# Kernel tuning notes

Hardware: AMD Instinct MI355X
Metric: run time of the kernel (lower is better)

The kernel has to match this reference:

```python
import jax, jax.numpy as jnp
import numpy as np

D_MODEL = 256
N_LEVELS = 4
N_HEADS = 8
N_POINTS = 4
OFF_DIM = 32
D_HEAD = D_MODEL // N_HEADS
SHAPES = [(64, 64), (32, 32), (16, 16), (8, 8)]  # (H_l, W_l)
LEN_IN = sum(h * w for h, w in SHAPES)  # 5440
N_BATCH = 4
LEN_Q = LEN_IN


def _offset_bias_init():
    # replicates _reset_parameters grid_init for sampling_offsets_bias
    thetas = np.arange(N_HEADS, dtype=np.float32) * (2.0 * np.pi / N_HEADS)
    grid = np.stack([np.cos(thetas), np.sin(thetas)], -1)
    grid = grid / np.abs(grid).max(-1, keepdims=True)
    grid = np.tile(grid[:, None, None, :], (1, N_LEVELS, N_POINTS, 1))
    grid = grid * np.arange(1, N_POINTS + 1, dtype=np.float32)[None, None, :, None]
    return jnp.asarray(grid, jnp.float32)  # (H, L, K, 2)


def setup_inputs() -> dict:
    key = jax.random.key(0)
    ks = jax.random.split(key, 12)
    s = 0.02
    return {
        "query": jax.random.normal(ks[0], (N_BATCH, LEN_Q, D_MODEL), jnp.float32),
        "reference_points": jax.random.uniform(ks[1], (N_BATCH, LEN_Q, N_LEVELS, 2), jnp.float32),
        "input_flatten": jax.random.normal(ks[2], (N_BATCH, LEN_IN, D_MODEL), jnp.float32),
        "input_spatial_shapes": jnp.asarray(SHAPES, jnp.int32),
        "offset_embeds_W": jax.random.normal(ks[3], (N_HEADS * N_LEVELS * N_POINTS * OFF_DIM, D_MODEL), jnp.float32) * s,
        "sampling_offsets_W": jax.random.normal(ks[4], (N_HEADS, N_LEVELS, N_POINTS, OFF_DIM, 2), jnp.float32) * s,
        "sampling_offsets_b": _offset_bias_init(),
        "attn_W": jax.random.normal(ks[5], (N_HEADS, N_LEVELS, N_POINTS, OFF_DIM, 1), jnp.float32) * s,
        "attn_b": jax.random.normal(ks[6], (N_HEADS, N_LEVELS, N_POINTS), jnp.float32) * s,
        "value_W": jax.random.normal(ks[7], (D_MODEL, D_MODEL), jnp.float32) * (1.0 / np.sqrt(D_MODEL)),
        "value_b": jnp.zeros((D_MODEL,), jnp.float32),
        "out_W": jax.random.normal(ks[8], (D_MODEL, D_MODEL), jnp.float32) * (1.0 / np.sqrt(D_MODEL)),
        "out_b": jnp.zeros((D_MODEL,), jnp.float32),
    }


def _bilinear(v, loc, H, W):
    # v: (N, heads, H*W, d_head); loc: (N, Lq, heads, K, 2) in [0,1] (x=width, y=height)
    # matches torch grid_sample(mode=bilinear, padding=zeros, align_corners=False)
    N, Lq, Hh, K, _ = loc.shape
    x = loc[..., 0] * W - 0.5
    y = loc[..., 1] * H - 0.5
    x0 = jnp.floor(x)
    y0 = jnp.floor(y)
    wx = (x - x0).transpose(0, 2, 1, 3).reshape(N, Hh, Lq * K)[..., None]
    wy = (y - y0).transpose(0, 2, 1, 3).reshape(N, Hh, Lq * K)[..., None]
    x0i = x0.astype(jnp.int32)
    y0i = y0.astype(jnp.int32)

    def gather(xi, yi):
        valid = (xi >= 0) & (xi < W) & (yi >= 0) & (yi < H)
        idx = jnp.clip(yi, 0, H - 1) * W + jnp.clip(xi, 0, W - 1)
        idx = idx.transpose(0, 2, 1, 3).reshape(N, Hh, Lq * K)
        g = jnp.take_along_axis(v, idx[..., None], axis=2)  # (N, heads, Lq*K, d)
        m = valid.transpose(0, 2, 1, 3).reshape(N, Hh, Lq * K)
        return g * m[..., None].astype(v.dtype)

    g00 = gather(x0i, y0i)
    g01 = gather(x0i + 1, y0i)
    g10 = gather(x0i, y0i + 1)
    g11 = gather(x0i + 1, y0i + 1)
    out = (g00 * (1 - wx) * (1 - wy) + g01 * wx * (1 - wy)
           + g10 * (1 - wx) * wy + g11 * wx * wy)
    return out.reshape(N, Hh, Lq, K, -1)  # (N, heads, Lq, K, d_head)


def _forward(query, reference_points, input_flatten,
             offset_embeds_W, sampling_offsets_W, sampling_offsets_b,
             attn_W, attn_b, value_W, value_b, out_W, out_b):
    N, Lq, _ = query.shape
    # value projection
    value = input_flatten @ value_W.T + value_b                      # (N, Lin, C)
    value = value.reshape(N, -1, N_HEADS, D_HEAD)                    # (N, Lin, H, d)

    # offset embedding + activation (offset_act_name == 'silu')
    oe = jax.nn.silu(query @ offset_embeds_W.T)                      # (N, Lq, H*L*K*off)
    oe = oe.reshape(N, Lq, N_HEADS, N_LEVELS, N_POINTS, OFF_DIM)

    offs = jnp.einsum('bqhlkd,hlkdc->bqhlkc', oe, sampling_offsets_W) + sampling_offsets_b
    aw = jnp.einsum('bqhlkd,hlkd->bqhlk', oe, attn_W[..., 0]) + attn_b
    aw = jax.nn.softmax(aw.reshape(N, Lq, N_HEADS, N_LEVELS * N_POINTS), axis=-1)
    aw = aw.reshape(N, Lq, N_HEADS, N_LEVELS, N_POINTS)

    # normalize offsets by (W_l, H_l) and add reference points (2-dim branch)
    normalizer = jnp.asarray([[w, h] for h, w in SHAPES], jnp.float32)  # (L, 2)
    loc = reference_points[:, :, None, :, None, :] + offs / normalizer[None, None, None, :, None, :]

    out = jnp.zeros((N, Lq, N_HEADS, D_HEAD), jnp.float32)
    start = 0
    for lvl, (H, W) in enumerate(SHAPES):
        v_l = value[:, start:start + H * W].transpose(0, 2, 1, 3)    # (N, heads, HW, d)
        sampled = _bilinear(v_l, loc[:, :, :, lvl], H, W)            # (N, heads, Lq, K, d)
        out = out + jnp.einsum('bhqkd,bqhk->bqhd', sampled, aw[:, :, :, lvl])
        start += H * W
    out = out.reshape(N, Lq, D_MODEL)
    return out @ out_W.T + out_b


def reference(query, reference_points, input_flatten, input_spatial_shapes,
              offset_embeds_W, sampling_offsets_W, sampling_offsets_b,
              attn_W, attn_b, value_W, value_b, out_W, out_b):
    # input_spatial_shapes matches SHAPES (static pyramid)
    return _forward(query, reference_points, input_flatten,
                    offset_embeds_W, sampling_offsets_W, sampling_offsets_b,
                    attn_W, attn_b, value_W, value_b, out_W, out_b)
```

## Files before the change

### kernel.cpp

```cpp
#include <hip/hip_runtime.h>
#include <hip/hip_bf16.h>

#define NB 4
#define LQ 5440
#define DM 256
#define NH 8
#define NL 4
#define NP 4
#define OFFD 32
#define DH 32
#define MTOT (NB * LQ)
#define OEN (NH * NL * NP * OFFD)
#define NGRP (NH * NL * NP)

typedef __attribute__((ext_vector_type(8))) short bf16x8;
typedef __attribute__((ext_vector_type(4))) float f32x4;
typedef unsigned int u32;

#define GLOAD_LDS16(gp, lp) \
    __builtin_amdgcn_global_load_lds((const __attribute__((address_space(1))) u32*)(gp), \
                                     (__attribute__((address_space(3))) u32*)(lp), 16, 0, 0)

__device__ __forceinline__ float bf2f(unsigned short u) {
    union { unsigned int i; float f; } v; v.i = ((unsigned int)u) << 16; return v.f;
}
__device__ __forceinline__ unsigned short f2bf(float x) {
    u32 u = __float_as_uint(x);
    u = u + 0x7fffu + ((u >> 16) & 1u);
    return (unsigned short)(u >> 16);
}
__device__ __forceinline__ u32 pk2(float a, float b) {
    u32 ua = __float_as_uint(a), ub = __float_as_uint(b);
    ua = ua + 0x7fffu + ((ua >> 16) & 1u);
    ub = ub + 0x7fffu + ((ub >> 16) & 1u);
    return (ua >> 16) | (ub & 0xffff0000u);
}
__device__ __forceinline__ float silu(float x) {
    float e = __expf(-x);
    return x * __builtin_amdgcn_rcpf(1.0f + e);
}

__global__ __launch_bounds__(256) void k_cvt2(
    const float* __restrict__ A, unsigned short* __restrict__ Ao,
    const float* __restrict__ B, unsigned short* __restrict__ Bo, int n4)
{
    int i = blockIdx.x * 256 + threadIdx.x;
    if (i >= n4) return;
    const float* src = blockIdx.y ? B : A;
    unsigned short* dst = blockIdx.y ? Bo : Ao;
    float4 v = *(const float4*)(src + (size_t)i * 4);
    ushort4 o;
    o.x = f2bf(v.x); o.y = f2bf(v.y); o.z = f2bf(v.z); o.w = f2bf(v.w);
    *(ushort4*)(dst + (size_t)i * 4) = o;
}
__global__ __launch_bounds__(256) void k_cvt3(
    const float* __restrict__ A, unsigned short* __restrict__ Ao, int nA4,
    const float* __restrict__ B, unsigned short* __restrict__ Bo, int nB4,
    const float* __restrict__ C, unsigned short* __restrict__ Co, int nC4,
    const float* __restrict__ SW, const float* __restrict__ AW,
    unsigned short* __restrict__ Rb)
{
    int i = blockIdx.x * 256 + threadIdx.x;
    if (blockIdx.y == 3) {
        if (i < 65536) {
            int gg = i >> 9, jo = (i >> 5) & 15, d = i & 31;
            float v = 0.f;
            if (jo == 0)      v = SW[(gg * 32 + d) * 2 + 0];
            else if (jo == 1) v = SW[(gg * 32 + d) * 2 + 1];
            else if (jo == 2) v = AW[gg * 32 + d];
            Rb[i] = f2bf(v);
        }
        return;
    }
    const float* src; unsigned short* dst; int n4;
    if (blockIdx.y == 0)      { src = A; dst = Ao; n4 = nA4; }
    else if (blockIdx.y == 1) { src = B; dst = Bo; n4 = nB4; }
    else                      { src = C; dst = Co; n4 = nC4; }
    if (i >= n4) return;
    float4 v = *(const float4*)(src + (size_t)i * 4);
    ushort4 o;
    o.x = f2bf(v.x); o.y = f2bf(v.y); o.z = f2bf(v.z); o.w = f2bf(v.w);
    *(ushort4*)(dst + (size_t)i * 4) = o;
}

__global__ __launch_bounds__(256) void k_oe_mfma(
    const unsigned short* __restrict__ Qb,
    const unsigned short* __restrict__ Wb,
    const unsigned short* __restrict__ Rb,
    const float* __restrict__ SB,
    const float* __restrict__ AB,
    float* __restrict__ offs_out,
    float* __restrict__ aw_out)
{
    __shared__ short sA[128 * 64];
    __shared__ short sB[128 * 64];
    int tid = threadIdx.x;
    int n0 = blockIdx.x * 128;
    int m0 = blockIdx.y * 128;

    int lane = tid & 63;
    int w = tid >> 6;
    int wA = w >> 1;
    int wB = w & 1;
    int lcol = lane & 15, quad = lane >> 4;

    int srow = tid >> 3;
    int sq = (tid & 7) ^ (srow & 7);
    const short* gA = (const short*)Qb + (size_t)(m0 + srow) * 256 + sq * 8;
    const short* gB = (const short*)Wb + (size_t)(n0 + srow) * 256 + sq * 8;
    short* lA = sA + w * 512;
    short* lB = sB + w * 512;

    f32x4 acc[4][4] = {};

    const short* pq = sA + (wB * 64 + lcol) * 64;
    const short* pw = sB + (wA * 64 + lcol) * 64;
    int rx7 = lcol & 7;
    int qa0 = (quad ^ rx7) * 8;
    int qa1 = ((4 + quad) ^ rx7) * 8;

    for (int kc = 0; kc < 256; kc += 64) {
#pragma unroll
        for (int j = 0; j < 4; j++) {
            GLOAD_LDS16(gA + kc + j * 32 * 256, lA + j * 2048);
            GLOAD_LDS16(gB + kc + j * 32 * 256, lB + j * 2048);
        }
        __syncthreads();
        bf16x8 a[4][2], b[4][2];
#pragma unroll
        for (int i = 0; i < 4; i++) {
            a[i][0] = *(const bf16x8*)(pw + i * 16 * 64 + qa0);
            a[i][1] = *(const bf16x8*)(pw + i * 16 * 64 + qa1);
            b[i][0] = *(const bf16x8*)(pq + i * 16 * 64 + qa0);
            b[i][1] = *(const bf16x8*)(pq + i * 16 * 64 + qa1);
        }
#pragma unroll
        for (int kh = 0; kh < 2; kh++)
#pragma unroll
            for (int i = 0; i < 4; i++)
#pragma unroll
                for (int j = 0; j < 4; j++)
                    acc[i][j] = __builtin_amdgcn_mfma_f32_16x16x32_bf16(
                        a[i][kh], b[j][kh], acc[i][j], 0, 0, 0);
        __syncthreads();
    }

    u32 ps[4][4][2];
#pragma unroll
    for (int i = 0; i < 4; i++)
#pragma unroll
        for (int j = 0; j < 4; j++) {
            ps[i][j][0] = pk2(silu(acc[i][j][0]), silu(acc[i][j][1]));
            ps[i][j][1] = pk2(silu(acc[i][j][2]), silu(acc[i][j][3]));
        }

    int srcbase = (quad & 1) * 32 + lcol;
    bool hi = quad >= 2;
    f32x4 zero = {};
#pragma unroll
    for (int g = 0; g < 2; g++) {
        int gg = (n0 + wA * 64 + g * 32) >> 5;
        bf16x8 afrag = *(const bf16x8*)(Rb + ((size_t)(gg * 16 + lcol) * 32 + quad * 8));
        float sb0 = SB[gg * 2 + 0], sb1 = SB[gg * 2 + 1], ab = AB[gg];
#pragma unroll
        for (int j = 0; j < 4; j++) {
            union { u32 u[4]; bf16x8 v; } bf;
#pragma unroll
            for (int b = 0; b < 2; b++) {
                int s = srcbase + b * 16;
#pragma unroll
                for (int c = 0; c < 2; c++) {
                    u32 x0 = (u32)__shfl((int)ps[2 * g + 0][j][c], s);
                    u32 x1 = (u32)__shfl((int)ps[2 * g + 1][j][c], s);
                    bf.u[b * 2 + c] = hi ? x1 : x0;
                }
            }
            f32x4 d2 = __builtin_amdgcn_mfma_f32_16x16x32_bf16(afrag, bf.v, zero, 0, 0, 0);
            if (quad == 0) {
                int m = m0 + wB * 64 + j * 16 + lcol;
                size_t oi = ((size_t)m * NGRP + gg) * 2;
                offs_out[oi + 0] = d2[0] + sb0;
                offs_out[oi + 1] = d2[1] + sb1;
                aw_out[(size_t)m * NGRP + gg] = d2[2] + ab;
            }
        }
    }
}

__global__ __launch_bounds__(256) void k_value_mfma(
    const unsigned short* __restrict__ Xb,
    const unsigned short* __restrict__ Wvb,
    const float* __restrict__ bias,
    unsigned short* __restrict__ Vtb)
{
    __shared__ short sA[128 * 64];
    __shared__ short sB[128 * 64];
    int tid = threadIdx.x;
    int n0 = blockIdx.x * 128;
    int m0 = blockIdx.y * 128;
    int lane = tid & 63;
    int w = tid >> 6;
    int wA = w >> 1;
    int wB = w & 1;
    int lcol = lane & 15, quad = lane >> 4;

    int srow = tid >> 3;
    int sq = (tid & 7) ^ (srow & 7);
    const short* gA = (const short*)Xb + (size_t)(m0 + srow) * 256 + sq * 8;
    const short* gB = (const short*)Wvb + (size_t)(n0 + srow) * 256 + sq * 8;
    short* lA = sA + w * 512;
    short* lB = sB + w * 512;

    f32x4 acc[4][4] = {};
    const short* px = sA + (wB * 64 + lcol) * 64;
    const short* pw = sB + (wA * 64 + lcol) * 64;
    int rx7 = lcol & 7;
    int qa0 = (quad ^ rx7) * 8;
    int qa1 = ((4 + quad) ^ rx7) * 8;

    for (int kc = 0; kc < 256; kc += 64) {
#pragma unroll
        for (int j = 0; j < 4; j++) {
            GLOAD_LDS16(gA + kc + j * 32 * 256, lA + j * 2048);
            GLOAD_LDS16(gB + kc + j * 32 * 256, lB + j * 2048);
        }
        __syncthreads();
        bf16x8 a[4][2], b[4][2];
#pragma unroll
        for (int i = 0; i < 4; i++) {
            a[i][0] = *(const bf16x8*)(pw + i * 16 * 64 + qa0);
            a[i][1] = *(const bf16x8*)(pw + i * 16 * 64 + qa1);
            b[i][0] = *(const bf16x8*)(px + i * 16 * 64 + qa0);
            b[i][1] = *(const bf16x8*)(px + i * 16 * 64 + qa1);
        }
#pragma unroll
        for (int kh = 0; kh < 2; kh++)
#pragma unroll
            for (int i = 0; i < 4; i++)
#pragma unroll
                for (int j = 0; j < 4; j++)
                    acc[i][j] = __builtin_amdgcn_mfma_f32_16x16x32_bf16(
                        a[i][kh], b[j][kh], acc[i][j], 0, 0, 0);
        __syncthreads();
    }

#pragma unroll
    for (int i = 0; i < 4; i++) {
        int nb = n0 + wA * 64 + i * 16 + quad * 4;
        int h = nb >> 5, db = nb & 31;
        float4 b4 = *(const float4*)&bias[nb];
#pragma unroll
        for (int j = 0; j < 4; j++) {
            int m = m0 + wB * 64 + j * 16 + lcol;
            int b = m / LQ, q = m - b * LQ;
            u32 lo = pk2(acc[i][j][0] + b4.x, acc[i][j][1] + b4.y);
            u32 hi2 = pk2(acc[i][j][2] + b4.z, acc[i][j][3] + b4.w);
            char* dst = (char*)Vtb + ((((size_t)b * NH + h) * LQ + q) * DH + db) * 2;
            *(uint2*)dst = make_uint2(lo, hi2);
        }
    }
}

__global__ __launch_bounds__(256) void k_out_mfma(
    const unsigned short* __restrict__ Xb,
    const unsigned short* __restrict__ Wob,
    const float* __restrict__ bias,
    float* __restrict__ Out)
{
    __shared__ short sA[128 * 64];
    __shared__ short sB[128 * 64];
    int tid = threadIdx.x;
    int n0 = blockIdx.x * 128;
    int m0 = blockIdx.y * 128;
    int lane = tid & 63;
    int w = tid >> 6;
    int wm = w >> 1, wn = w & 1;
    int lcol = lane & 15, lrow = lane >> 4;

    int srow = tid >> 3;
    int sq = (tid & 7) ^ (srow & 7);
    const short* gA = (const short*)Xb + (size_t)(m0 + srow) * 256 + sq * 8;
    const short* gB = (const short*)Wob + (size_t)(n0 + srow) * 256 + sq * 8;
    short* lA = sA + w * 512;
    short* lB = sB + w * 512;

    f32x4 acc[4][4] = {};
    const short* pa = sA + (wm * 64 + lcol) * 64;
    const short* pb = sB + (wn * 64 + lcol) * 64;
    int rx7 = lcol & 7;
    int qa0 = (lrow ^ rx7) * 8;
    int qa1 = ((4 + lrow) ^ rx7) * 8;

    for (int kc = 0; kc < 256; kc += 64) {
#pragma unroll
        for (int j = 0; j < 4; j++) {
            GLOAD_LDS16(gA + kc + j * 32 * 256, lA + j * 2048);
            GLOAD_LDS16(gB + kc + j * 32 * 256, lB + j * 2048);
        }
        __syncthreads();
        bf16x8 a[4][2], b[4][2];
#pragma unroll
        for (int i = 0; i < 4; i++) {
            a[i][0] = *(const bf16x8*)(pa + i * 16 * 64 + qa0);
            a[i][1] = *(const bf16x8*)(pa + i * 16 * 64 + qa1);
            b[i][0] = *(const bf16x8*)(pb + i * 16 * 64 + qa0);
            b[i][1] = *(const bf16x8*)(pb + i * 16 * 64 + qa1);
        }
#pragma unroll
        for (int kh = 0; kh < 2; kh++)
#pragma unroll
            for (int mi = 0; mi < 4; mi++)
#pragma unroll
                for (int ni = 0; ni < 4; ni++)
                    acc[mi][ni] = __builtin_amdgcn_mfma_f32_16x16x32_bf16(
                        a[mi][kh], b[ni][kh], acc[mi][ni], 0, 0, 0);
        __syncthreads();
    }

#pragma unroll
    for (int mi = 0; mi < 4; mi++) {
#pragma unroll
        for (int ni = 0; ni < 4; ni++) {
            int n = n0 + wn * 64 + ni * 16 + lcol;
            float bn = bias[n];
#pragma unroll
            for (int r = 0; r < 4; r++) {
                int m = m0 + wm * 64 + mi * 16 + lrow * 4 + r;
                Out[(size_t)m * 256 + n] = acc[mi][ni][r] + bn;
            }
        }
    }
}

__global__ __launch_bounds__(256) void k_sample(
    const unsigned short* __restrict__ Vtb,
    const float* __restrict__ refp,
    const float* __restrict__ offs,
    const float* __restrict__ awl,
    unsigned short* __restrict__ atnb)
{
    int tid = threadIdx.x;
    int m_base = blockIdx.x * 4;
    __shared__ int2 s_iw[4][128][4];

#pragma unroll
    for (int rep = 0; rep < 2; rep++) {
        int p = tid & 127;
        int mloc = (tid >> 7) + rep * 2;
        int m = m_base + mloc;
        int l = (p >> 2) & 3;
        float logit = awl[(size_t)m * 128 + p];
        float mx = logit;
#pragma unroll
        for (int off = 1; off < 16; off <<= 1) mx = fmaxf(mx, __shfl_xor(mx, off));
        float e = __expf(logit - mx);
        float s = e;
#pragma unroll
        for (int off = 1; off < 16; off <<= 1) s += __shfl_xor(s, off);
        float prob = e * __builtin_amdgcn_rcpf(s);

        float ox = offs[((size_t)m * 128 + p) * 2 + 0];
        float oy = offs[((size_t)m * 128 + p) * 2 + 1];
        float rx = refp[(size_t)m * 8 + l * 2 + 0];
        float ry = refp[(size_t)m * 8 + l * 2 + 1];
        int Wl = 64 >> l;
        int base = (l == 0) ? 0 : (l == 1) ? 4096 : (l == 2) ? 5120 : 5376;
        float fW = (float)Wl;
        float x = rx * fW + ox - 0.5f;
        float y = ry * fW + oy - 0.5f;
        float x0f = floorf(x), y0f = floorf(y);
        float wx = x - x0f, wy = y - y0f;
        int x0 = (int)x0f, y0 = (int)y0f;
        int xc0 = min(max(x0, 0), Wl - 1), xc1 = min(max(x0 + 1, 0), Wl - 1);
        int yc0 = min(max(y0, 0), Wl - 1), yc1 = min(max(y0 + 1, 0), Wl - 1);
        float vx0 = (x0 >= 0 && x0 < Wl) ? 1.f : 0.f;
        float vx1 = (x0 + 1 < Wl) ? 1.f : 0.f;
        float vy0 = (y0 >= 0 && y0 < Wl) ? 1.f : 0.f;
        float vy1 = (y0 + 1 < Wl) ? 1.f : 0.f;
        if (x0 + 1 < 0) vx1 = 0.f;
        if (y0 + 1 < 0) vy1 = 0.f;
        s_iw[mloc][p][0] = make_int2((base + yc0 * Wl + xc0) * 64,
                                     __float_as_int(prob * (1.f - wx) * (1.f - wy) * vx0 * vy0));
        s_iw[mloc][p][1] = make_int2((base + yc0 * Wl + xc1) * 64,
                                     __float_as_int(prob * wx * (1.f - wy) * vx1 * vy0));
        s_iw[mloc][p][2] = make_int2((base + yc1 * Wl + xc0) * 64,
                                     __float_as_int(prob * (1.f - wx) * wy * vx0 * vy1));
        s_iw[mloc][p][3] = make_int2((base + yc1 * Wl + xc1) * 64,
                                     __float_as_int(prob * wx * wy * vx1 * vy1));
    }
    __syncthreads();

    int wv = tid >> 6, lane = tid & 63;
    int p8 = lane >> 3, seg = lane & 7;
    int m = m_base + wv;
    int b = m / LQ;
    const char* vB = (const char*)(Vtb + (size_t)b * NH * LQ * DH) + seg * 8;
#pragma unroll
    for (int h = 0; h < 8; h++) {
        const char* ph = vB + (size_t)h * (LQ * DH * 2);
        float a0 = 0.f, a1 = 0.f, a2 = 0.f, a3 = 0.f;
#pragma unroll
        for (int pg = 0; pg < 2; pg++) {
            int p = h * 16 + pg * 8 + p8;
#pragma unroll
            for (int c = 0; c < 4; c++) {
                int2 iw = s_iw[wv][p][c];
                uint2 v = *(const uint2*)(ph + iw.x);
                float wgt = __int_as_float(iw.y);
                a0 += wgt * __uint_as_float(v.x << 16);
                a1 += wgt * __uint_as_float(v.x & 0xffff0000u);
                a2 += wgt * __uint_as_float(v.y << 16);
                a3 += wgt * __uint_as_float(v.y & 0xffff0000u);
            }
        }
#pragma unroll
        for (int off = 8; off <= 32; off <<= 1) {
            a0 += __shfl_xor(a0, off);
            a1 += __shfl_xor(a1, off);
            a2 += __shfl_xor(a2, off);
            a3 += __shfl_xor(a3, off);
        }
        if (p8 == 0) {
            ((uint2*)atnb)[(size_t)m * 64 + h * 8 + seg] =
                make_uint2(pk2(a0, a1), pk2(a2, a3));
        }
    }
}

extern "C" void kernel_launch(void* const* d_in, const int* in_sizes, int n_in,
                              void* d_out, int out_size, void* d_ws, size_t ws_size,
                              hipStream_t stream) {
    const float* query  = (const float*)d_in[0];
    const float* refp   = (const float*)d_in[1];
    const float* inflat = (const float*)d_in[2];
    const float* We  = (const float*)d_in[4];
    const float* SW  = (const float*)d_in[5];
    const float* SB  = (const float*)d_in[6];
    const float* AWw = (const float*)d_in[7];
    const float* ABb = (const float*)d_in[8];
    const float* VW  = (const float*)d_in[9];
    const float* Vb  = (const float*)d_in[10];
    const float* OW  = (const float*)d_in[11];
    const float* Ob  = (const float*)d_in[12];
    float* out = (float*)d_out;

    float* ws = (float*)d_ws;
    unsigned short* Vtb  = (unsigned short*)ws;
    float* offs          = ws + 2785280;
    float* awl           = offs + 5570560;
    unsigned short* Qbf  = (unsigned short*)(awl + 2785280);
    unsigned short* Webf = Qbf + 5570560;
    unsigned short* Xbf  = Webf + 1048576;
    unsigned short* Wvbf = Xbf + 5570560;
    unsigned short* OWbf = Wvbf + 65536;
    unsigned short* Rbf  = OWbf + 65536;
    unsigned short* atnb = Xbf;

    k_cvt2<<<dim3(5440, 2), 256, 0, stream>>>(query, Qbf, inflat, Xbf, MTOT * 256 / 4);
    k_cvt3<<<dim3(1024, 4), 256, 0, stream>>>(We, Webf, OEN * 256 / 4,
                                              VW, Wvbf, 256 * 256 / 4,
                                              OW, OWbf, 256 * 256 / 4,
                                              SW, AWw, Rbf);

    k_value_mfma<<<dim3(2, MTOT / 128), 256, 0, stream>>>(Xbf, Wvbf, Vb, Vtb);

    k_oe_mfma<<<dim3(OEN / 128, MTOT / 128), 256, 0, stream>>>(
        Qbf, Webf, Rbf, SB, ABb, offs, awl);

    k_sample<<<dim3(MTOT / 4), 256, 0, stream>>>(Vtb, refp, offs, awl, atnb);

    k_out_mfma<<<dim3(2, MTOT / 128), 256, 0, stream>>>(atnb, OWbf, Ob, out);
}
```

Before: 251.6 us.

## Register-prefetch GEMM tiles instead of direct global-to-LDS loads

In the three MFMA GEMM kernels, direct global_load_lds transfers are replaced with register prefetching. The next K-chunk is loaded into VGPRs while the current chunk is computed, then written to LDS between barriers, and the trailing barrier is dropped. The aim is to overlap global memory latency with MFMA work, at the cost of more registers and an explicit LDS store pass. The sampling kernel's shared index/weight array is also padded from 4 to 5 entries, likely to reduce LDS bank conflicts.

```diff
diff --git a/kernel.cpp b/kernel.cpp
--- a/kernel.cpp
+++ b/kernel.cpp
@@ -16,10 +16,6 @@
 typedef __attribute__((ext_vector_type(8))) short bf16x8;
 typedef __attribute__((ext_vector_type(4))) float f32x4;
 typedef unsigned int u32;
-
-#define GLOAD_LDS16(gp, lp) \
-    __builtin_amdgcn_global_load_lds((const __attribute__((address_space(1))) u32*)(gp), \
-                                     (__attribute__((address_space(3))) u32*)(lp), 16, 0, 0)
 
 __device__ __forceinline__ float bf2f(unsigned short u) {
     union { unsigned int i; float f; } v; v.i = ((unsigned int)u) << 16; return v.f;
@@ -83,6 +79,7 @@
     *(ushort4*)(dst + (size_t)i * 4) = o;
 }
 
+
 __global__ __launch_bounds__(256) void k_oe_mfma(
     const unsigned short* __restrict__ Qb,
     const unsigned short* __restrict__ Wb,
@@ -108,8 +105,6 @@
     int sq = (tid & 7) ^ (srow & 7);
     const short* gA = (const short*)Qb + (size_t)(m0 + srow) * 256 + sq * 8;
     const short* gB = (const short*)Wb + (size_t)(n0 + srow) * 256 + sq * 8;
-    short* lA = sA + w * 512;
-    short* lB = sB + w * 512;
 
     f32x4 acc[4][4] = {};
 
@@ -119,11 +114,29 @@
     int qa0 = (quad ^ rx7) * 8;
     int qa1 = ((4 + quad) ^ rx7) * 8;
 
-    for (int kc = 0; kc < 256; kc += 64) {
+    uint4 ra[4], rb2[4];
+#pragma unroll
+    for (int j = 0; j < 4; j++) {
+        ra[j]  = *(const uint4*)(gA + j * 32 * 256);
+        rb2[j] = *(const uint4*)(gB + j * 32 * 256);
+    }
+#pragma unroll
+    for (int it = 0; it < 4; it++) {
+        uint4 na[4], nb[4];
+        if (it < 3) {
+            const short* qA = gA + (it + 1) * 64;
+            const short* qB = gB + (it + 1) * 64;
+#pragma unroll
+            for (int j = 0; j < 4; j++) {
+                na[j] = *(const uint4*)(qA + j * 32 * 256);
+                nb[j] = *(const uint4*)(qB + j * 32 * 256);
+            }
+        }
+        __syncthreads();
 #pragma unroll
         for (int j = 0; j < 4; j++) {
-            GLOAD_LDS16(gA + kc + j * 32 * 256, lA + j * 2048);
-            GLOAD_LDS16(gB + kc + j * 32 * 256, lB + j * 2048);
+            *(uint4*)((char*)sA + j * 4096 + tid * 16) = ra[j];
+            *(uint4*)((char*)sB + j * 4096 + tid * 16) = rb2[j];
         }
         __syncthreads();
         bf16x8 a[4][2], b[4][2];
@@ -142,7 +155,10 @@
                 for (int j = 0; j < 4; j++)
                     acc[i][j] = __builtin_amdgcn_mfma_f32_16x16x32_bf16(
                         a[i][kh], b[j][kh], acc[i][j], 0, 0, 0);
-        __syncthreads();
+        if (it < 3) {
+#pragma unroll
+            for (int j = 0; j < 4; j++) { ra[j] = na[j]; rb2[j] = nb[j]; }
+        }
     }
 
     u32 ps[4][4][2];
@@ -208,8 +224,6 @@
     int sq = (tid & 7) ^ (srow & 7);
     const short* gA = (const short*)Xb + (size_t)(m0 + srow) * 256 + sq * 8;
     const short* gB = (const short*)Wvb + (size_t)(n0 + srow) * 256 + sq * 8;
-    short* lA = sA + w * 512;
-    short* lB = sB + w * 512;
 
     f32x4 acc[4][4] = {};
     const short* px = sA + (wB * 64 + lcol) * 64;
@@ -218,11 +232,29 @@
     int qa0 = (quad ^ rx7) * 8;
     int qa1 = ((4 + quad) ^ rx7) * 8;
 
-    for (int kc = 0; kc < 256; kc += 64) {
+    uint4 ra[4], rb2[4];
+#pragma unroll
+    for (int j = 0; j < 4; j++) {
+        ra[j]  = *(const uint4*)(gA + j * 32 * 256);
+        rb2[j] = *(const uint4*)(gB + j * 32 * 256);
+    }
+#pragma unroll
+    for (int it = 0; it < 4; it++) {
+        uint4 na[4], nb[4];
+        if (it < 3) {
+            const short* qA = gA + (it + 1) * 64;
+            const short* qB = gB + (it + 1) * 64;
+#pragma unroll
+            for (int j = 0; j < 4; j++) {
+                na[j] = *(const uint4*)(qA + j * 32 * 256);
+                nb[j] = *(const uint4*)(qB + j * 32 * 256);
+            }
+        }
+        __syncthreads();
 #pragma unroll
         for (int j = 0; j < 4; j++) {
-            GLOAD_LDS16(gA + kc + j * 32 * 256, lA + j * 2048);
-            GLOAD_LDS16(gB + kc + j * 32 * 256, lB + j * 2048);
+            *(uint4*)((char*)sA + j * 4096 + tid * 16) = ra[j];
+            *(uint4*)((char*)sB + j * 4096 + tid * 16) = rb2[j];
         }
         __syncthreads();
         bf16x8 a[4][2], b[4][2];
@@ -241,14 +273,17 @@
                 for (int j = 0; j < 4; j++)
                     acc[i][j] = __builtin_amdgcn_mfma_f32_16x16x32_bf16(
                         a[i][kh], b[j][kh], acc[i][j], 0, 0, 0);
-        __syncthreads();
+        if (it < 3) {
+#pragma unroll
+            for (int j = 0; j < 4; j++) { ra[j] = na[j]; rb2[j] = nb[j]; }
+        }
     }
 
 #pragma unroll
     for (int i = 0; i < 4; i++) {
-        int nb = n0 + wA * 64 + i * 16 + quad * 4;
-        int h = nb >> 5, db = nb & 31;
-        float4 b4 = *(const float4*)&bias[nb];
+        int nb4 = n0 + wA * 64 + i * 16 + quad * 4;
+        int h = nb4 >> 5, db = nb4 & 31;
+        float4 b4 = *(const float4*)&bias[nb4];
 #pragma unroll
         for (int j = 0; j < 4; j++) {
             int m = m0 + wB * 64 + j * 16 + lcol;
@@ -281,8 +316,6 @@
     int sq = (tid & 7) ^ (srow & 7);
     const short* gA = (const short*)Xb + (size_t)(m0 + srow) * 256 + sq * 8;
     const short* gB = (const short*)Wob + (size_t)(n0 + srow) * 256 + sq * 8;
-    short* lA = sA + w * 512;
-    short* lB = sB + w * 512;
 
     f32x4 acc[4][4] = {};
     const short* pa = sA + (wm * 64 + lcol) * 64;
@@ -291,11 +324,29 @@
     int qa0 = (lrow ^ rx7) * 8;
     int qa1 = ((4 + lrow) ^ rx7) * 8;
 
-    for (int kc = 0; kc < 256; kc += 64) {
+    uint4 ra[4], rb2[4];
+#pragma unroll
+    for (int j = 0; j < 4; j++) {
+        ra[j]  = *(const uint4*)(gA + j * 32 * 256);
+        rb2[j] = *(const uint4*)(gB + j * 32 * 256);
+    }
+#pragma unroll
+    for (int it = 0; it < 4; it++) {
+        uint4 na[4], nb[4];
+        if (it < 3) {
+            const short* qA = gA + (it + 1) * 64;
+            const short* qB = gB + (it + 1) * 64;
+#pragma unroll
+            for (int j = 0; j < 4; j++) {
+                na[j] = *(const uint4*)(qA + j * 32 * 256);
+                nb[j] = *(const uint4*)(qB + j * 32 * 256);
+            }
+        }
+        __syncthreads();
 #pragma unroll
         for (int j = 0; j < 4; j++) {
-            GLOAD_LDS16(gA + kc + j * 32 * 256, lA + j * 2048);
-            GLOAD_LDS16(gB + kc + j * 32 * 256, lB + j * 2048);
+            *(uint4*)((char*)sA + j * 4096 + tid * 16) = ra[j];
+            *(uint4*)((char*)sB + j * 4096 + tid * 16) = rb2[j];
         }
         __syncthreads();
         bf16x8 a[4][2], b[4][2];
@@ -314,7 +365,10 @@
                 for (int ni = 0; ni < 4; ni++)
                     acc[mi][ni] = __builtin_amdgcn_mfma_f32_16x16x32_bf16(
                         a[mi][kh], b[ni][kh], acc[mi][ni], 0, 0, 0);
-        __syncthreads();
+        if (it < 3) {
+#pragma unroll
+            for (int j = 0; j < 4; j++) { ra[j] = na[j]; rb2[j] = nb[j]; }
+        }
     }
 
 #pragma unroll
@@ -341,7 +395,7 @@
 {
     int tid = threadIdx.x;
     int m_base = blockIdx.x * 4;
-    __shared__ int2 s_iw[4][128][4];
+    __shared__ int2 s_iw[4][128][5];
 
 #pragma unroll
     for (int rep = 0; rep < 2; rep++) {
```

Measured after the change: 589.1 us. 2.34x slower.

## Split sampling kernel across heads with a second grid dimension

Applied to the files above, without the earlier changes.

The sampling kernel now launches one block per group of four queries and per head, where before one block handled all eight heads in a loop. Each wave computes the 16 sampling indices and weights for its own head only, which gives eight times as many smaller blocks with shorter per-thread work. The cost is that only 16 of 64 lanes do the softmax and index setup, and more blocks each pay launch and __syncthreads overhead. The boundary-validity checks are also folded into a single expression, which is equivalent to the old code.

```diff
diff --git a/kernel.cpp b/kernel.cpp
--- a/kernel.cpp
+++ b/kernel.cpp
@@ -82,6 +82,7 @@
     o.x = f2bf(v.x); o.y = f2bf(v.y); o.z = f2bf(v.z); o.w = f2bf(v.w);
     *(ushort4*)(dst + (size_t)i * 4) = o;
 }
+
 
 __global__ __launch_bounds__(256) void k_oe_mfma(
     const unsigned short* __restrict__ Qb,
@@ -246,9 +247,9 @@
 
 #pragma unroll
     for (int i = 0; i < 4; i++) {
-        int nb = n0 + wA * 64 + i * 16 + quad * 4;
-        int h = nb >> 5, db = nb & 31;
-        float4 b4 = *(const float4*)&bias[nb];
+        int nb4 = n0 + wA * 64 + i * 16 + quad * 4;
+        int h = nb4 >> 5, db = nb4 & 31;
+        float4 b4 = *(const float4*)&bias[nb4];
 #pragma unroll
         for (int j = 0; j < 4; j++) {
             int m = m0 + wB * 64 + j * 16 + lcol;
@@ -340,15 +341,16 @@
     unsigned short* __restrict__ atnb)
 {
     int tid = threadIdx.x;
+    int h = blockIdx.y;
     int m_base = blockIdx.x * 4;
-    __shared__ int2 s_iw[4][128][4];
-
-#pragma unroll
-    for (int rep = 0; rep < 2; rep++) {
-        int p = tid & 127;
-        int mloc = (tid >> 7) + rep * 2;
-        int m = m_base + mloc;
-        int l = (p >> 2) & 3;
+    int wv = tid >> 6, lane = tid & 63;
+    int m = m_base + wv;
+    __shared__ int2 s_iw[4][16][5];
+
+    if (lane < 16) {
+        int idx16 = lane;
+        int p = h * 16 + idx16;
+        int l = idx16 >> 2;
         float logit = awl[(size_t)m * 128 + p];
         float mx = logit;
 #pragma unroll
@@ -374,56 +376,48 @@
         int xc0 = min(max(x0, 0), Wl - 1), xc1 = min(max(x0 + 1, 0), Wl - 1);
         int yc0 = min(max(y0, 0), Wl - 1), yc1 = min(max(y0 + 1, 0), Wl - 1);
         float vx0 = (x0 >= 0 && x0 < Wl) ? 1.f : 0.f;
-        float vx1 = (x0 + 1 < Wl) ? 1.f : 0.f;
+        float vx1 = (x0 + 1 >= 0 && x0 + 1 < Wl) ? 1.f : 0.f;
         float vy0 = (y0 >= 0 && y0 < Wl) ? 1.f : 0.f;
-        float vy1 = (y0 + 1 < Wl) ? 1.f : 0.f;
-        if (x0 + 1 < 0) vx1 = 0.f;
-        if (y0 + 1 < 0) vy1 = 0.f;
-        s_iw[mloc][p][0] = make_int2((base + yc0 * Wl + xc0) * 64,
-                                     __float_as_int(prob * (1.f - wx) * (1.f - wy) * vx0 * vy0));
-        s_iw[mloc][p][1] = make_int2((base + yc0 * Wl + xc1) * 64,
-                                     __float_as_int(prob * wx * (1.f - wy) * vx1 * vy0));
-        s_iw[mloc][p][2] = make_int2((base + yc1 * Wl + xc0) * 64,
-                                     __float_as_int(prob * (1.f - wx) * wy * vx0 * vy1));
-        s_iw[mloc][p][3] = make_int2((base + yc1 * Wl + xc1) * 64,
-                                     __float_as_int(prob * wx * wy * vx1 * vy1));
+        float vy1 = (y0 + 1 >= 0 && y0 + 1 < Wl) ? 1.f : 0.f;
+        s_iw[wv][idx16][0] = make_int2((base + yc0 * Wl + xc0) * 64,
+                                       __float_as_int(prob * (1.f - wx) * (1.f - wy) * vx0 * vy0));
+        s_iw[wv][idx16][1] = make_int2((base + yc0 * Wl + xc1) * 64,
+                                       __float_as_int(prob * wx * (1.f - wy) * vx1 * vy0));
+        s_iw[wv][idx16][2] = make_int2((base + yc1 * Wl + xc0) * 64,
+                                       __float_as_int(prob * (1.f - wx) * wy * vx0 * vy1));
+        s_iw[wv][idx16][3] = make_int2((base + yc1 * Wl + xc1) * 64,
+                                       __float_as_int(prob * wx * wy * vx1 * vy1));
     }
     __syncthreads();
 
-    int wv = tid >> 6, lane = tid & 63;
     int p8 = lane >> 3, seg = lane & 7;
-    int m = m_base + wv;
     int b = m / LQ;
-    const char* vB = (const char*)(Vtb + (size_t)b * NH * LQ * DH) + seg * 8;
-#pragma unroll
-    for (int h = 0; h < 8; h++) {
-        const char* ph = vB + (size_t)h * (LQ * DH * 2);
-        float a0 = 0.f, a1 = 0.f, a2 = 0.f, a3 = 0.f;
-#pragma unroll
-        for (int pg = 0; pg < 2; pg++) {
-            int p = h * 16 + pg * 8 + p8;
-#pragma unroll
-            for (int c = 0; c < 4; c++) {
-                int2 iw = s_iw[wv][p][c];
-                uint2 v = *(const uint2*)(ph + iw.x);
-                float wgt = __int_as_float(iw.y);
-                a0 += wgt * __uint_as_float(v.x << 16);
-                a1 += wgt * __uint_as_float(v.x & 0xffff0000u);
-                a2 += wgt * __uint_as_float(v.y << 16);
-                a3 += wgt * __uint_as_float(v.y & 0xffff0000u);
-            }
-        }
-#pragma unroll
-        for (int off = 8; off <= 32; off <<= 1) {
-            a0 += __shfl_xor(a0, off);
-            a1 += __shfl_xor(a1, off);
-            a2 += __shfl_xor(a2, off);
-            a3 += __shfl_xor(a3, off);
-        }
-        if (p8 == 0) {
-            ((uint2*)atnb)[(size_t)m * 64 + h * 8 + seg] =
-                make_uint2(pk2(a0, a1), pk2(a2, a3));
-        }
+    const char* ph = (const char*)(Vtb + ((size_t)b * NH + h) * LQ * DH) + seg * 8;
+    float a0 = 0.f, a1 = 0.f, a2 = 0.f, a3 = 0.f;
+#pragma unroll
+    for (int pg = 0; pg < 2; pg++) {
+        int pt = pg * 8 + p8;
+#pragma unroll
+        for (int c = 0; c < 4; c++) {
+            int2 iw = s_iw[wv][pt][c];
+            uint2 v = *(const uint2*)(ph + iw.x);
+            float wgt = __int_as_float(iw.y);
+            a0 += wgt * __uint_as_float(v.x << 16);
+            a1 += wgt * __uint_as_float(v.x & 0xffff0000u);
+            a2 += wgt * __uint_as_float(v.y << 16);
+            a3 += wgt * __uint_as_float(v.y & 0xffff0000u);
+        }
+    }
+#pragma unroll
+    for (int off = 8; off <= 32; off <<= 1) {
+        a0 += __shfl_xor(a0, off);
+        a1 += __shfl_xor(a1, off);
+        a2 += __shfl_xor(a2, off);
+        a3 += __shfl_xor(a3, off);
+    }
+    if (p8 == 0) {
+        ((uint2*)atnb)[(size_t)m * 64 + h * 8 + seg] =
+            make_uint2(pk2(a0, a1), pk2(a2, a3));
     }
 }
 
@@ -467,7 +461,7 @@
     k_oe_mfma<<<dim3(OEN / 128, MTOT / 128), 256, 0, stream>>>(
         Qbf, Webf, Rbf, SB, ABb, offs, awl);
 
-    k_sample<<<dim3(MTOT / 4), 256, 0, stream>>>(Vtb, refp, offs, awl, atnb);
+    k_sample<<<dim3(MTOT / 4, NH), 256, 0, stream>>>(Vtb, refp, offs, awl, atnb);
 
     k_out_mfma<<<dim3(2, MTOT / 128), 256, 0, stream>>>(atnb, OWbf, Ob, out);
 }
```

After: 282.8 us. +12.4%, slower.
